# Kernel tuning notes

Hardware: AMD Instinct MI355X
Metric: run time of the kernel (lower is better)

## Reference

```python
import jax, jax.numpy as jnp
import numpy as np

# OGB full_atom_feature_dims
FEAT_DIMS = np.array([119, 5, 12, 12, 10, 6, 6, 2, 2], dtype=np.int32)
OFFSETS = jnp.asarray(np.concatenate([[0], np.cumsum(FEAT_DIMS)[:-1]]), dtype=jnp.int32)  # [9]
TOTAL_ROWS = int(FEAT_DIMS.sum())  # 174
DIM = 256
N_CLASS = 10
B, MAX_NODE = 128, 1024


def setup_inputs() -> dict:
    key = jax.random.key(0)
    ks = jax.random.split(key, 16)
    # per-field valid categorical indices, stacked -> [B, MAX_NODE, 9]
    cols = [jax.random.randint(ks[i], (B, MAX_NODE), 0, int(FEAT_DIMS[i]), dtype=jnp.int32)
            for i in range(9)]
    node_feat = jnp.stack(cols, axis=-1)
    num_nodes = jax.random.randint(ks[9], (B,), 1, MAX_NODE + 1, dtype=jnp.int32)
    rxn_class = jax.random.randint(ks[10], (B,), 0, N_CLASS, dtype=jnp.int32)
    # learned params
    atom_emb = jax.random.normal(ks[11], (TOTAL_ROWS, DIM), dtype=jnp.float32) * 0.02
    rxn_emb = jax.random.normal(ks[12], (N_CLASS, DIM), dtype=jnp.float32) * 0.02
    lin_w = jax.random.normal(ks[13], (DIM, 2 * DIM), dtype=jnp.float32) * (1.0 / np.sqrt(2 * DIM))
    lin_b = jax.random.normal(ks[14], (DIM,), dtype=jnp.float32) * 0.01
    return {"node_feat": node_feat, "num_nodes": num_nodes, "rxn_class": rxn_class,
            "atom_emb": atom_emb, "rxn_emb": rxn_emb, "lin_w": lin_w, "lin_b": lin_b}


def reference(node_feat, num_nodes, rxn_class, atom_emb, rxn_emb, lin_w, lin_b):
    # AtomEncoder: sum of 9 per-field embedding lookups (tables concatenated with offsets)
    idx = node_feat + OFFSETS  # [B, N, 9]
    enc = atom_emb[idx].sum(axis=2)  # [B, N, dim]
    # zero-pad positions beyond num_nodes (ragged-to-dense scatter)
    mask = (jnp.arange(MAX_NODE)[None, :] < num_nodes[:, None])[..., None]  # [B, N, 1]
    enc = jnp.where(mask, enc, jnp.zeros((), dtype=enc.dtype))
    # class embedding broadcast over all node slots (including padding, as in original)
    cls = jnp.broadcast_to(rxn_emb[rxn_class][:, None, :], enc.shape)  # [B, N, dim]
    h = jnp.concatenate([enc, cls], axis=-1)  # [B, N, 2*dim]
    out = jnp.einsum('bnd,od->bno', h, lin_w) + lin_b  # [B, N, dim]
    return out
```

## Files before the change

### kernel.cpp

```cpp
#include <hip/hip_runtime.h>
#include <stdint.h>

#define BATCH 128
#define MAXN 1024
#define NF 9
#define DIM 256
#define NCLS 10

#define BASE1 119
#define BASE2 179
#define BASE3 299
#define QROWS 443

typedef __attribute__((ext_vector_type(4))) float f32x4;
typedef __attribute__((ext_vector_type(2))) uint32_t u32x2;

__device__ __forceinline__ ushort f32_to_bf16_rne(float x) {
  uint32_t u = __float_as_uint(x);
  u += 0x7fffu + ((u >> 16) & 1u);
  return (ushort)(u >> 16);
}

__device__ __forceinline__ f32x4 bf4_to_f32x4(u32x2 v) {
  f32x4 r;
  r.x = __uint_as_float(v.x << 16);
  r.y = __uint_as_float(v.x & 0xffff0000u);
  r.z = __uint_as_float(v.y << 16);
  r.w = __uint_as_float(v.y & 0xffff0000u);
  return r;
}

__global__ __launch_bounds__(256) void prep_kernel(
    const float* __restrict__ rxn_emb, const float* __restrict__ lin_w,
    const float* __restrict__ lin_b, const float* __restrict__ atom_emb,
    ushort* __restrict__ Qb, float* __restrict__ clsT)
{
  __shared__ float S[4][DIM];
  const int bid = blockIdx.x;
  const int t = threadIdx.x;
  const bool isCls = bid < 3;
  const int row0 = isCls ? bid * 4 : (bid - 3) * 4;
  const int rmax = isCls ? NCLS : QROWS;
  const int nrows = (rmax - row0 < 4) ? (rmax - row0) : 4;

#pragma unroll
  for (int r = 0; r < 4; ++r) {
    float v = 0.f;
    if (r < nrows) {
      const int q = row0 + r;
      if (isCls) {
        v = rxn_emb[q * DIM + t];
      } else if (q < BASE1) {
        v = atom_emb[q * DIM + t];
      } else if (q < BASE2) {
        int x = q - BASE1;
        v = atom_emb[(119 + x / 12) * DIM + t] + atom_emb[(124 + x % 12) * DIM + t];
      } else if (q < BASE3) {
        int x = q - BASE2;
        v = atom_emb[(136 + x / 10) * DIM + t] + atom_emb[(148 + x % 10) * DIM + t];
      } else {
        int x = q - BASE3;
        int i8 = x & 1, i7 = (x >> 1) & 1, y = x >> 2;
        v = atom_emb[(158 + y / 6) * DIM + t] + atom_emb[(164 + y % 6) * DIM + t]
          + atom_emb[(170 + i7) * DIM + t] + atom_emb[(172 + i8) * DIM + t];
      }
    }
    S[r][t] = v;
  }
  __syncthreads();

  const float* wrow = lin_w + (size_t)t * 2 * DIM + (isCls ? DIM : 0);
  const float init = isCls ? lin_b[t] : 0.f;
  float a0 = init, a1 = init, a2 = init, a3 = init;
#pragma unroll 4
  for (int d = 0; d < DIM; d += 4) {
    float4 w4 = *(const float4*)(wrow + d);
    a0 += w4.x * S[0][d] + w4.y * S[0][d + 1] + w4.z * S[0][d + 2] + w4.w * S[0][d + 3];
    a1 += w4.x * S[1][d] + w4.y * S[1][d + 1] + w4.z * S[1][d + 2] + w4.w * S[1][d + 3];
    a2 += w4.x * S[2][d] + w4.y * S[2][d + 1] + w4.z * S[2][d + 2] + w4.w * S[2][d + 3];
    a3 += w4.x * S[3][d] + w4.y * S[3][d + 1] + w4.z * S[3][d + 2] + w4.w * S[3][d + 3];
  }
  if (isCls) {
    if (0 < nrows) clsT[(row0 + 0) * DIM + t] = a0;
    if (1 < nrows) clsT[(row0 + 1) * DIM + t] = a1;
    if (2 < nrows) clsT[(row0 + 2) * DIM + t] = a2;
    if (3 < nrows) clsT[(row0 + 3) * DIM + t] = a3;
  } else {
    if (0 < nrows) Qb[(row0 + 0) * DIM + t] = f32_to_bf16_rne(a0);
    if (1 < nrows) Qb[(row0 + 1) * DIM + t] = f32_to_bf16_rne(a1);
    if (2 < nrows) Qb[(row0 + 2) * DIM + t] = f32_to_bf16_rne(a2);
    if (3 < nrows) Qb[(row0 + 3) * DIM + t] = f32_to_bf16_rne(a3);
  }
}

__global__ __launch_bounds__(256, 8) void main_kernel(
    const int* __restrict__ node_feat, const int* __restrict__ num_nodes,
    const int* __restrict__ rxn_class,
    const ushort* __restrict__ Qb, const float* __restrict__ clsT,
    float* __restrict__ out)
{
  const int tid = threadIdx.x;
  const int lane = tid & 63;
  const int w = __builtin_amdgcn_readfirstlane(tid >> 6);
  const int wid = blockIdx.x * 4 + w;
  const int b = wid >> 7;
  const int n0 = (wid & 127) << 3;
  const int nn = num_nodes[b];

  const f32x4 cf = ((const f32x4*)clsT)[rxn_class[b] * 64 + lane];
  f32x4* __restrict__ outp = (f32x4*)out + ((size_t)(b * MAXN + n0)) * 64 + lane;

  if (n0 >= nn) {
#pragma unroll
    for (int i = 0; i < 8; ++i)
      outp[i * 64] = cf;
    return;
  }

  const int* __restrict__ p = node_feat + (size_t)(b * MAXN + n0) * NF;
  const u32x2* __restrict__ Q2 = (const u32x2*)Qb;

  if (n0 + 8 <= nn) {
#pragma unroll 4
    for (int i = 0; i < 8; ++i) {
      const int j0 = p[i * NF + 0];
      const int j1 = BASE1 + p[i * NF + 1] * 12 + p[i * NF + 2];
      const int j2 = BASE2 + p[i * NF + 3] * 10 + p[i * NF + 4];
      const int j3 = BASE3 + ((p[i * NF + 5] * 6 + p[i * NF + 6]) * 2 + p[i * NF + 7]) * 2 + p[i * NF + 8];
      const u32x2 v0 = Q2[j0 * 64 + lane];
      const u32x2 v1 = Q2[j1 * 64 + lane];
      const u32x2 v2 = Q2[j2 * 64 + lane];
      const u32x2 v3 = Q2[j3 * 64 + lane];
      const f32x4 s = (bf4_to_f32x4(v0) + bf4_to_f32x4(v1))
                    + (bf4_to_f32x4(v2) + bf4_to_f32x4(v3));
      outp[i * 64] = cf + s;
    }
    return;
  }

#pragma unroll 4
  for (int i = 0; i < 8; ++i) {
    const int j0 = p[i * NF + 0];
    const int j1 = BASE1 + p[i * NF + 1] * 12 + p[i * NF + 2];
    const int j2 = BASE2 + p[i * NF + 3] * 10 + p[i * NF + 4];
    const int j3 = BASE3 + ((p[i * NF + 5] * 6 + p[i * NF + 6]) * 2 + p[i * NF + 7]) * 2 + p[i * NF + 8];
    const u32x2 v0 = Q2[j0 * 64 + lane];
    const u32x2 v1 = Q2[j1 * 64 + lane];
    const u32x2 v2 = Q2[j2 * 64 + lane];
    const u32x2 v3 = Q2[j3 * 64 + lane];
    const float m = (n0 + i < nn) ? 1.f : 0.f;
    const f32x4 s = (bf4_to_f32x4(v0) + bf4_to_f32x4(v1))
                  + (bf4_to_f32x4(v2) + bf4_to_f32x4(v3));
    outp[i * 64] = cf + m * s;
  }
}

extern "C" void kernel_launch(void* const* d_in, const int* in_sizes, int n_in,
                              void* d_out, int out_size, void* d_ws, size_t ws_size,
                              hipStream_t stream) {
  const int* node_feat = (const int*)d_in[0];
  const int* num_nodes = (const int*)d_in[1];
  const int* rxn_class = (const int*)d_in[2];
  const float* atom_emb = (const float*)d_in[3];
  const float* rxn_emb = (const float*)d_in[4];
  const float* lin_w = (const float*)d_in[5];
  const float* lin_b = (const float*)d_in[6];
  float* outp = (float*)d_out;

  ushort* Qb = (ushort*)d_ws;
  float* clsT = (float*)((char*)d_ws + QROWS * DIM * sizeof(ushort));

  prep_kernel<<<3 + (QROWS + 3) / 4, 256, 0, stream>>>(rxn_emb, lin_w, lin_b,
                                                       atom_emb, Qb, clsT);
  main_kernel<<<4096, 256, 0, stream>>>(node_feat, num_nodes, rxn_class,
                                        Qb, clsT, outp);
}
```

Baseline: 42.94 us.

## Precompute packed gather indices in prep kernel and double nodes per wave

The prep kernel gains extra blocks that read the 9 raw node features per node and write four precombined row indices as one int4 into workspace. The main kernel then loads one int4 per node instead of nine scalar ints, and each wave now handles 16 nodes instead of 8, with half as many blocks and no occupancy hint in the launch bounds. This is meant to shorten the dependent index-load chain in the main kernel. In exchange it adds a 2 MB write and read of packed indices plus a larger prep launch, and the relaxed launch bounds may lower occupancy.

```diff
diff --git a/kernel.cpp b/kernel.cpp
--- a/kernel.cpp
+++ b/kernel.cpp
@@ -11,6 +11,9 @@
 #define BASE2 179
 #define BASE3 299
 #define QROWS 443
+
+#define TBLK 114
+#define PACKBLK (BATCH * MAXN / 256)
 
 typedef __attribute__((ext_vector_type(4))) float f32x4;
 typedef __attribute__((ext_vector_type(2))) uint32_t u32x2;
@@ -33,11 +36,25 @@
 __global__ __launch_bounds__(256) void prep_kernel(
     const float* __restrict__ rxn_emb, const float* __restrict__ lin_w,
     const float* __restrict__ lin_b, const float* __restrict__ atom_emb,
-    ushort* __restrict__ Qb, float* __restrict__ clsT)
+    const int* __restrict__ node_feat,
+    ushort* __restrict__ Qb, float* __restrict__ clsT, int4* __restrict__ jpack)
 {
-  __shared__ float S[4][DIM];
   const int bid = blockIdx.x;
   const int t = threadIdx.x;
+
+  if (bid >= TBLK) {
+    const int node = (bid - TBLK) * 256 + t;
+    const int* p = node_feat + (size_t)node * NF;
+    int4 jv;
+    jv.x = p[0];
+    jv.y = BASE1 + p[1] * 12 + p[2];
+    jv.z = BASE2 + p[3] * 10 + p[4];
+    jv.w = BASE3 + ((p[5] * 6 + p[6]) * 2 + p[7]) * 2 + p[8];
+    jpack[node] = jv;
+    return;
+  }
+
+  __shared__ float S[4][DIM];
   const bool isCls = bid < 3;
   const int row0 = isCls ? bid * 4 : (bid - 3) * 4;
   const int rmax = isCls ? NCLS : QROWS;
@@ -93,8 +110,8 @@
   }
 }
 
-__global__ __launch_bounds__(256, 8) void main_kernel(
-    const int* __restrict__ node_feat, const int* __restrict__ num_nodes,
+__global__ __launch_bounds__(256) void main_kernel(
+    const int4* __restrict__ jpack, const int* __restrict__ num_nodes,
     const int* __restrict__ rxn_class,
     const ushort* __restrict__ Qb, const float* __restrict__ clsT,
     float* __restrict__ out)
@@ -103,8 +120,8 @@
   const int lane = tid & 63;
   const int w = __builtin_amdgcn_readfirstlane(tid >> 6);
   const int wid = blockIdx.x * 4 + w;
-  const int b = wid >> 7;
-  const int n0 = (wid & 127) << 3;
+  const int b = wid >> 6;
+  const int n0 = (wid & 63) << 4;
   const int nn = num_nodes[b];
 
   const f32x4 cf = ((const f32x4*)clsT)[rxn_class[b] * 64 + lane];
@@ -112,25 +129,22 @@
 
   if (n0 >= nn) {
 #pragma unroll
-    for (int i = 0; i < 8; ++i)
+    for (int i = 0; i < 16; ++i)
       outp[i * 64] = cf;
     return;
   }
 
-  const int* __restrict__ p = node_feat + (size_t)(b * MAXN + n0) * NF;
+  const int4* __restrict__ jp = jpack + (size_t)b * MAXN + n0;
   const u32x2* __restrict__ Q2 = (const u32x2*)Qb;
 
-  if (n0 + 8 <= nn) {
-#pragma unroll 4
-    for (int i = 0; i < 8; ++i) {
-      const int j0 = p[i * NF + 0];
-      const int j1 = BASE1 + p[i * NF + 1] * 12 + p[i * NF + 2];
-      const int j2 = BASE2 + p[i * NF + 3] * 10 + p[i * NF + 4];
-      const int j3 = BASE3 + ((p[i * NF + 5] * 6 + p[i * NF + 6]) * 2 + p[i * NF + 7]) * 2 + p[i * NF + 8];
-      const u32x2 v0 = Q2[j0 * 64 + lane];
-      const u32x2 v1 = Q2[j1 * 64 + lane];
-      const u32x2 v2 = Q2[j2 * 64 + lane];
-      const u32x2 v3 = Q2[j3 * 64 + lane];
+  if (n0 + 16 <= nn) {
+#pragma unroll 8
+    for (int i = 0; i < 16; ++i) {
+      const int4 jv = jp[i];
+      const u32x2 v0 = Q2[jv.x * 64 + lane];
+      const u32x2 v1 = Q2[jv.y * 64 + lane];
+      const u32x2 v2 = Q2[jv.z * 64 + lane];
+      const u32x2 v3 = Q2[jv.w * 64 + lane];
       const f32x4 s = (bf4_to_f32x4(v0) + bf4_to_f32x4(v1))
                     + (bf4_to_f32x4(v2) + bf4_to_f32x4(v3));
       outp[i * 64] = cf + s;
@@ -138,16 +152,13 @@
     return;
   }
 
-#pragma unroll 4
-  for (int i = 0; i < 8; ++i) {
-    const int j0 = p[i * NF + 0];
-    const int j1 = BASE1 + p[i * NF + 1] * 12 + p[i * NF + 2];
-    const int j2 = BASE2 + p[i * NF + 3] * 10 + p[i * NF + 4];
-    const int j3 = BASE3 + ((p[i * NF + 5] * 6 + p[i * NF + 6]) * 2 + p[i * NF + 7]) * 2 + p[i * NF + 8];
-    const u32x2 v0 = Q2[j0 * 64 + lane];
-    const u32x2 v1 = Q2[j1 * 64 + lane];
-    const u32x2 v2 = Q2[j2 * 64 + lane];
-    const u32x2 v3 = Q2[j3 * 64 + lane];
+#pragma unroll 8
+  for (int i = 0; i < 16; ++i) {
+    const int4 jv = jp[i];
+    const u32x2 v0 = Q2[jv.x * 64 + lane];
+    const u32x2 v1 = Q2[jv.y * 64 + lane];
+    const u32x2 v2 = Q2[jv.z * 64 + lane];
+    const u32x2 v3 = Q2[jv.w * 64 + lane];
     const float m = (n0 + i < nn) ? 1.f : 0.f;
     const f32x4 s = (bf4_to_f32x4(v0) + bf4_to_f32x4(v1))
                   + (bf4_to_f32x4(v2) + bf4_to_f32x4(v3));
@@ -169,9 +180,11 @@
 
   ushort* Qb = (ushort*)d_ws;
   float* clsT = (float*)((char*)d_ws + QROWS * DIM * sizeof(ushort));
+  int4* jpack = (int4*)((char*)d_ws + 262144);
 
-  prep_kernel<<<3 + (QROWS + 3) / 4, 256, 0, stream>>>(rxn_emb, lin_w, lin_b,
-                                                       atom_emb, Qb, clsT);
-  main_kernel<<<4096, 256, 0, stream>>>(node_feat, num_nodes, rxn_class,
+  prep_kernel<<<TBLK + PACKBLK, 256, 0, stream>>>(rxn_emb, lin_w, lin_b,
+                                                  atom_emb, node_feat,
+                                                  Qb, clsT, jpack);
+  main_kernel<<<2048, 256, 0, stream>>>(jpack, num_nodes, rxn_class,
                                         Qb, clsT, outp);
 }
```

After: 44.92 us. +4.6%, slower.

## Split padding fill into separate kernel and trim partial-tile gather loop

Applied to the files above, without the earlier changes.

Moves the writes of the class-only padding rows out of the gather kernel into a dedicated fill kernel that streams contiguous output from each batch's num_nodes onward. The gather kernel now exits early for fully padded tiles, and in partial tiles it loops only over valid nodes instead of masking. This aims to balance work and make the padding stores contiguous, at the cost of an extra kernel launch and dropping the occupancy hint on the gather kernel. The prep grid size is now a named constant with the same value.

```diff
diff --git a/kernel.cpp b/kernel.cpp
--- a/kernel.cpp
+++ b/kernel.cpp
@@ -11,6 +11,7 @@
 #define BASE2 179
 #define BASE3 299
 #define QROWS 443
+#define TBLK 114
 
 typedef __attribute__((ext_vector_type(4))) float f32x4;
 typedef __attribute__((ext_vector_type(2))) uint32_t u32x2;
@@ -93,7 +94,22 @@
   }
 }
 
-__global__ __launch_bounds__(256, 8) void main_kernel(
+__global__ __launch_bounds__(256) void fill_kernel(
+    const int* __restrict__ num_nodes, const int* __restrict__ rxn_class,
+    const float* __restrict__ clsT, float* __restrict__ out)
+{
+  const int b = blockIdx.x >> 3;
+  const int k = blockIdx.x & 7;
+  const int t = threadIdx.x;
+  const int nn = num_nodes[b];
+  const f32x4 cf = ((const f32x4*)clsT)[rxn_class[b] * 64 + (t & 63)];
+  f32x4* __restrict__ out4 = (f32x4*)out;
+  const size_t end = ((size_t)b * MAXN + MAXN) * 64;
+  for (size_t i = ((size_t)b * MAXN + nn) * 64 + k * 256 + t; i < end; i += 2048)
+    out4[i] = cf;
+}
+
+__global__ __launch_bounds__(256) void gather_kernel(
     const int* __restrict__ node_feat, const int* __restrict__ num_nodes,
     const int* __restrict__ rxn_class,
     const ushort* __restrict__ Qb, const float* __restrict__ clsT,
@@ -107,16 +123,10 @@
   const int n0 = (wid & 127) << 3;
   const int nn = num_nodes[b];
 
+  if (n0 >= nn) return;
+
   const f32x4 cf = ((const f32x4*)clsT)[rxn_class[b] * 64 + lane];
   f32x4* __restrict__ outp = (f32x4*)out + ((size_t)(b * MAXN + n0)) * 64 + lane;
-
-  if (n0 >= nn) {
-#pragma unroll
-    for (int i = 0; i < 8; ++i)
-      outp[i * 64] = cf;
-    return;
-  }
-
   const int* __restrict__ p = node_feat + (size_t)(b * MAXN + n0) * NF;
   const u32x2* __restrict__ Q2 = (const u32x2*)Qb;
 
@@ -138,8 +148,8 @@
     return;
   }
 
-#pragma unroll 4
-  for (int i = 0; i < 8; ++i) {
+  const int lim = nn - n0;
+  for (int i = 0; i < lim; ++i) {
     const int j0 = p[i * NF + 0];
     const int j1 = BASE1 + p[i * NF + 1] * 12 + p[i * NF + 2];
     const int j2 = BASE2 + p[i * NF + 3] * 10 + p[i * NF + 4];
@@ -148,10 +158,9 @@
     const u32x2 v1 = Q2[j1 * 64 + lane];
     const u32x2 v2 = Q2[j2 * 64 + lane];
     const u32x2 v3 = Q2[j3 * 64 + lane];
-    const float m = (n0 + i < nn) ? 1.f : 0.f;
     const f32x4 s = (bf4_to_f32x4(v0) + bf4_to_f32x4(v1))
                   + (bf4_to_f32x4(v2) + bf4_to_f32x4(v3));
-    outp[i * 64] = cf + m * s;
+    outp[i * 64] = cf + s;
   }
 }
 
@@ -170,8 +179,9 @@
   ushort* Qb = (ushort*)d_ws;
   float* clsT = (float*)((char*)d_ws + QROWS * DIM * sizeof(ushort));
 
-  prep_kernel<<<3 + (QROWS + 3) / 4, 256, 0, stream>>>(rxn_emb, lin_w, lin_b,
-                                                       atom_emb, Qb, clsT);
-  main_kernel<<<4096, 256, 0, stream>>>(node_feat, num_nodes, rxn_class,
-                                        Qb, clsT, outp);
+  prep_kernel<<<TBLK, 256, 0, stream>>>(rxn_emb, lin_w, lin_b, atom_emb,
+                                        Qb, clsT);
+  fill_kernel<<<BATCH * 8, 256, 0, stream>>>(num_nodes, rxn_class, clsT, outp);
+  gather_kernel<<<4096, 256, 0, stream>>>(node_feat, num_nodes, rxn_class,
+                                          Qb, clsT, outp);
 }
```

New measurement: 53.92 us. 1.26x slower.
